# Kernel tuning notes

Hardware: AMD Instinct MI355X
Metric: run time of the kernel (lower is better)

Reference implementation:

```python
import jax, jax.numpy as jnp
import numpy as np

B, T, C = 4, 2048, 2048
H, N = 32, 64          # num_heads, head_size
EPS = 1e-5 * 8.0 ** 2  # GroupNorm eps = 1e-5 * head_size_divisor**2


def setup_inputs() -> dict:
    key = jax.random.key(0)
    ks = jax.random.split(key, 20)
    f = lambda i, shape, s=0.02: jax.random.normal(ks[i], shape, jnp.float32) * s
    return {
        'hidden': jax.random.normal(ks[0], (B, T, C), jnp.float32),
        'time_maa_x': f(1, (C,)), 'time_maa_w': f(2, (C,)), 'time_maa_k': f(3, (C,)),
        'time_maa_v': f(4, (C,)), 'time_maa_r': f(5, (C,)), 'time_maa_g': f(6, (C,)),
        'time_maa_w1': f(7, (C, 160)), 'time_maa_w2': f(8, (5, 32, C)),
        'time_decay': f(9, (C,), 0.5), 'time_decay_w1': f(10, (C, 64)),
        'time_decay_w2': f(11, (64, C)),
        'time_faaaa': f(12, (H, N), 0.5),
        'w_r': f(13, (C, C)), 'w_k': f(14, (C, C)), 'w_v': f(15, (C, C)),
        'w_g': f(16, (C, C)), 'w_o': f(17, (C, C)),
        'ln_w': jnp.ones((C,), jnp.float32), 'ln_b': jnp.zeros((C,), jnp.float32),
    }


def reference(hidden, time_maa_x, time_maa_w, time_maa_k, time_maa_v, time_maa_r,
              time_maa_g, time_maa_w1, time_maa_w2, time_decay, time_decay_w1,
              time_decay_w2, time_faaaa, w_r, w_k, w_v, w_g, w_o, ln_w, ln_b):
    x = hidden
    # time_shift: prepend zero row, drop last (state=None path)
    shifted = jnp.pad(x, ((0, 0), (1, 0), (0, 0)))[:, :-1]
    xx = shifted - x
    # data-dependent low-rank token-shift interpolation (5 lerp channels)
    xm = x + xx * time_maa_x
    t5 = jnp.tanh(jnp.einsum('btc,ce->bte', xm, time_maa_w1)).reshape(B, T, 5, 32)
    m = jnp.einsum('btfe,fec->fbtc', t5, time_maa_w2)  # [5,B,T,C]
    mw, mk, mv, mr, mg = m[0], m[1], m[2], m[3], m[4]
    xd = x + xx * (time_maa_w + mw)
    xk = x + xx * (time_maa_k + mk)
    xv = x + xx * (time_maa_v + mv)
    xr = x + xx * (time_maa_r + mr)
    xg = x + xx * (time_maa_g + mg)
    r = xr @ w_r.T
    k = xk @ w_k.T
    v = xv @ w_v.T
    g = jax.nn.silu(xg @ w_g.T)
    td = time_decay + jnp.tanh(xd @ time_decay_w1) @ time_decay_w2  # [B,T,C]
    w = jnp.exp(-jnp.exp(td))  # per-channel decay in (0,1)
    # [B,T,C] -> [T,B,H,N] for the scan
    to_tbhn = lambda a: a.reshape(B, T, H, N).transpose(1, 0, 2, 3)
    rT, kT, vT, wT = to_tbhn(r), to_tbhn(k), to_tbhn(v), to_tbhn(w)
    u = time_faaaa  # [H,N]
    state0 = jnp.zeros((B, H, N, N), jnp.float32)  # [B,H,key,value]

    def step(state, ins):
        r_t, k_t, v_t, w_t = ins  # each [B,H,N]
        att = k_t[..., :, None] * v_t[..., None, :]        # outer product k v^T
        out_t = jnp.einsum('bhn,bhnm->bhm', r_t,
                           u[None, :, :, None] * att + state)
        new_state = att + w_t[..., None] * state           # decay along key dim
        return new_state, out_t

    _, outs = jax.lax.scan(step, state0, (rT, kT, vT, wT))  # outs [T,B,H,N]
    out = outs.transpose(1, 0, 2, 3)                         # [B,T,H,N]
    # GroupNorm with H groups over C channels, applied per (b,t) sample
    mu = out.mean(-1, keepdims=True)
    var = out.var(-1, keepdims=True)
    out = (out - mu) / jnp.sqrt(var + EPS)
    out = (out * ln_w.reshape(H, N) + ln_b.reshape(H, N)).reshape(B, T, C)
    out = out * g
    return out @ w_o.T
```

## Files before the change

kernel.cpp:

```cpp
#include <hip/hip_runtime.h>
#include <hip/hip_bf16.h>
#include <math.h>

typedef __hip_bfloat16 bf16;
typedef __attribute__((ext_vector_type(8))) short short8;
typedef __attribute__((ext_vector_type(4))) float f32x4;

#define Bb 4
#define Tt 2048
#define Cc 2048
#define Hh 32
#define Nn 64
#define BT (Bb*Tt)
#define Gg 16
#define Ll 128
#define SPLITK 8

__device__ __forceinline__ float b2f(bf16 x) { return __bfloat162float(x); }
__device__ __forceinline__ bf16  f2b(float x) { return __float2bfloat16(x); }

__global__ __launch_bounds__(256) void cvt_kernel(
    const float* __restrict__ in, bf16* __restrict__ out)
{
  int i = blockIdx.x * 256 + threadIdx.x;
  out[i] = f2b(in[i]);
}

__global__ __launch_bounds__(256) void cvt_t2_kernel(
    const float* __restrict__ in, bf16* __restrict__ hi, bf16* __restrict__ lo,
    int N)
{
  int idx = blockIdx.x * 256 + threadIdx.x;
  int n = idx >> 11, k = idx & 2047;
  float v = in[(size_t)k * N + n];
  bf16 h = f2b(v);
  hi[idx] = h;
  lo[idx] = f2b(v - b2f(h));
}

__global__ __launch_bounds__(256) void prep_xm_kernel(
    const float* __restrict__ x, const float* __restrict__ maa_x,
    bf16* __restrict__ xm)
{
  int idx = blockIdx.x * 256 + threadIdx.x;
  int c  = idx & (Cc - 1);
  int bt = idx >> 11;
  int t  = bt & (Tt - 1);
  float xv   = x[idx];
  float prev = (t == 0) ? 0.f : x[idx - Cc];
  xm[idx] = f2b(xv + (prev - xv) * maa_x[c]);
}

#define LDA 40

__global__ __launch_bounds__(256) void mfma_gemm_kernel(
    const bf16* __restrict__ A, const bf16* __restrict__ B,
    bf16* __restrict__ outB, float* __restrict__ outF, int mode)
{
  __shared__ bf16 As[128 * LDA];
  __shared__ bf16 Bs[128 * LDA];
  int tid  = threadIdx.x;
  int lane = tid & 63, wid = tid >> 6;
  int wm = wid & 1, wn = wid >> 1;
  int quad = lane >> 4, l16 = lane & 15;
  size_t rowBase = (size_t)blockIdx.x * 128;
  size_t colBase = (size_t)blockIdx.y * 128;

  f32x4 acc[4][4];
  #pragma unroll
  for (int i = 0; i < 4; ++i)
    #pragma unroll
    for (int j = 0; j < 4; ++j)
      acc[i][j] = (f32x4){0.f, 0.f, 0.f, 0.f};

  for (int k0 = 0; k0 < 2048; k0 += 32) {
    #pragma unroll
    for (int pass = 0; pass < 2; ++pass) {
      int chunk = tid + pass * 256;
      int row = chunk >> 2, kc = (chunk & 3) * 8;
      short8 av = *(const short8*)(A + (rowBase + row) * 2048 + k0 + kc);
      short8 bv = *(const short8*)(B + (colBase + row) * 2048 + k0 + kc);
      *(short8*)(As + row * LDA + kc) = av;
      *(short8*)(Bs + row * LDA + kc) = bv;
    }
    __syncthreads();
    short8 af[4], bf[4];
    #pragma unroll
    for (int i = 0; i < 4; ++i) {
      af[i] = *(const short8*)(As + (wm * 64 + i * 16 + l16) * LDA + quad * 8);
      bf[i] = *(const short8*)(Bs + (wn * 64 + i * 16 + l16) * LDA + quad * 8);
    }
    #pragma unroll
    for (int i = 0; i < 4; ++i)
      #pragma unroll
      for (int j = 0; j < 4; ++j)
        acc[i][j] = __builtin_amdgcn_mfma_f32_16x16x32_bf16(af[i], bf[j], acc[i][j], 0, 0, 0);
    __syncthreads();
  }

  #pragma unroll
  for (int i = 0; i < 4; ++i) {
    #pragma unroll
    for (int j = 0; j < 4; ++j) {
      int gc = colBase + wn * 64 + j * 16 + l16;
      #pragma unroll
      for (int reg = 0; reg < 4; ++reg) {
        int gr = rowBase + wm * 64 + i * 16 + quad * 4 + reg;
        float v = acc[i][j][reg];
        size_t idx = (size_t)gr * 2048 + gc;
        if (mode == 0)      outB[idx] = f2b(v);
        else if (mode == 2) outB[idx] = f2b(v / (1.f + expf(-v)));
        else                outF[idx] = v;
      }
    }
  }
}

template<int NF>
__global__ __launch_bounds__(256) void mfma_skinny_kernel(
    const bf16* __restrict__ A, const bf16* __restrict__ Bt_hi,
    const bf16* __restrict__ Bt_lo,
    float* __restrict__ partial, int kseg_len)
{
  constexpr int N = NF * 16;
  __shared__ bf16 As[64 * LDA];
  __shared__ bf16 Bs[2 * N * LDA];
  int tid = threadIdx.x;
  int lane = tid & 63, w = tid >> 6;
  int quad = lane >> 4, l16 = lane & 15;
  int rowBase = blockIdx.x * 64;
  int kbeg = blockIdx.y * kseg_len;

  f32x4 acc[NF];
  #pragma unroll
  for (int f = 0; f < NF; ++f) acc[f] = (f32x4){0.f, 0.f, 0.f, 0.f};

  for (int k0 = kbeg; k0 < kbeg + kseg_len; k0 += 32) {
    {
      int row = tid >> 2, kc = (tid & 3) * 8;
      *(short8*)(As + row * LDA + kc) =
          *(const short8*)(A + (size_t)(rowBase + row) * 2048 + k0 + kc);
    }
    for (int c = tid; c < N * 8; c += 256) {
      int half = c >= N * 4;
      int cc = c - half * N * 4;
      int row = cc >> 2, kc = (cc & 3) * 8;
      const bf16* src = half ? Bt_lo : Bt_hi;
      *(short8*)(Bs + (half * N + row) * LDA + kc) =
          *(const short8*)(src + (size_t)row * 2048 + k0 + kc);
    }
    __syncthreads();
    short8 af = *(const short8*)(As + (w * 16 + l16) * LDA + quad * 8);
    #pragma unroll
    for (int f = 0; f < NF; ++f) {
      short8 bh = *(const short8*)(Bs + (f * 16 + l16) * LDA + quad * 8);
      short8 bl = *(const short8*)(Bs + ((N + f * 16 + l16)) * LDA + quad * 8);
      acc[f] = __builtin_amdgcn_mfma_f32_16x16x32_bf16(af, bh, acc[f], 0, 0, 0);
      acc[f] = __builtin_amdgcn_mfma_f32_16x16x32_bf16(af, bl, acc[f], 0, 0, 0);
    }
    __syncthreads();
  }

  #pragma unroll
  for (int f = 0; f < NF; ++f) {
    int gc = f * 16 + l16;
    #pragma unroll
    for (int reg = 0; reg < 4; ++reg) {
      int gr = rowBase + w * 16 + quad * 4 + reg;
      partial[((size_t)blockIdx.y * 8192 + gr) * N + gc] = acc[f][reg];
    }
  }
}

__global__ __launch_bounds__(256) void reduce_tanh_kernel(
    const float* __restrict__ partial, bf16* __restrict__ out, int MN)
{
  int idx = blockIdx.x * 256 + threadIdx.x;
  float s = 0.f;
  #pragma unroll
  for (int j = 0; j < SPLITK; ++j) s += partial[(size_t)j * MN + idx];
  out[idx] = f2b(tanhf(s));
}

#define BM 128
#define BN 128
#define BKk 16

__global__ __launch_bounds__(256) void gemm_kernel(
    const bf16* __restrict__ A, const float* __restrict__ Bm,
    bf16* __restrict__ outB,
    const float* __restrict__ bias,
    int M, int N, int K, int transB, int mode)
{
  __shared__ float As[BKk][BM + 1];
  __shared__ float Bs[BKk][BN + 1];
  int tid = threadIdx.x;
  int rowBase = blockIdx.x * BM;
  int colBase = blockIdx.y * BN;
  int tx = tid & 15, ty = tid >> 4;
  float acc[8][8];
  #pragma unroll
  for (int i = 0; i < 8; ++i)
    #pragma unroll
    for (int j = 0; j < 8; ++j) acc[i][j] = 0.f;

  for (int k0 = 0; k0 < K; k0 += BKk) {
    #pragma unroll
    for (int i = 0; i < 8; ++i) {
      int lin = tid + i * 256;
      int r = lin >> 4, kk = lin & 15;
      int gr = rowBase + r, gk = k0 + kk;
      float val = 0.f;
      if (gr < M && gk < K) val = b2f(A[(size_t)gr * K + gk]);
      As[kk][r] = val;
    }
    #pragma unroll
    for (int i = 0; i < 8; ++i) {
      int lin = tid + i * 256;
      float val = 0.f;
      if (transB) {
        int n = lin >> 4, kk = lin & 15;
        int gn = colBase + n, gk = k0 + kk;
        if (gn < N && gk < K) val = Bm[(size_t)gn * K + gk];
        Bs[kk][n] = val;
      } else {
        int kk = lin >> 7, n = lin & 127;
        int gn = colBase + n, gk = k0 + kk;
        if (gn < N && gk < K) val = Bm[(size_t)gk * N + gn];
        Bs[kk][n] = val;
      }
    }
    __syncthreads();
    #pragma unroll
    for (int kk = 0; kk < BKk; ++kk) {
      float a[8], b[8];
      #pragma unroll
      for (int i = 0; i < 8; ++i) a[i] = As[kk][ty * 8 + i];
      #pragma unroll
      for (int j = 0; j < 8; ++j) b[j] = Bs[kk][tx * 8 + j];
      #pragma unroll
      for (int i = 0; i < 8; ++i)
        #pragma unroll
        for (int j = 0; j < 8; ++j)
          acc[i][j] = fmaf(a[i], b[j], acc[i][j]);
    }
    __syncthreads();
  }
  #pragma unroll
  for (int i = 0; i < 8; ++i) {
    int gr = rowBase + ty * 8 + i;
    if (gr >= M) continue;
    #pragma unroll
    for (int j = 0; j < 8; ++j) {
      int gn = colBase + tx * 8 + j;
      if (gn >= N) continue;
      float v = acc[i][j];
      size_t idx = (size_t)gr * N + gn;
      if (mode == 1)      outB[idx] = f2b(tanhf(v));
      else                outB[idx] = f2b(bias[gn] + v);
    }
  }
}

__global__ __launch_bounds__(256) void lerp5_kernel(
    const float* __restrict__ x, const bf16* __restrict__ t5,
    const float* __restrict__ w2,
    const float* __restrict__ maa_w, const float* __restrict__ maa_k,
    const float* __restrict__ maa_v, const float* __restrict__ maa_r,
    const float* __restrict__ maa_g,
    bf16* __restrict__ xd, bf16* __restrict__ xk, bf16* __restrict__ xv_,
    bf16* __restrict__ xr, bf16* __restrict__ xg)
{
  __shared__ float t5s[160];
  int bt   = blockIdx.x >> 3;
  int cblk = blockIdx.x & 7;
  int c = cblk * 256 + threadIdx.x;
  if (threadIdx.x < 160) t5s[threadIdx.x] = b2f(t5[(size_t)bt * 160 + threadIdx.x]);
  __syncthreads();
  int t = bt & (Tt - 1);
  size_t idx = (size_t)bt * Cc + c;
  float xv0  = x[idx];
  float prev = (t == 0) ? 0.f : x[idx - Cc];
  float xx = prev - xv0;
  float m[5];
  #pragma unroll
  for (int f = 0; f < 5; ++f) {
    float s = 0.f;
    #pragma unroll
    for (int e = 0; e < 32; ++e)
      s = fmaf(t5s[f * 32 + e], w2[(size_t)(f * 32 + e) * Cc + c], s);
    m[f] = s;
  }
  xd[idx]  = f2b(xv0 + xx * (maa_w[c] + m[0]));
  xk[idx]  = f2b(xv0 + xx * (maa_k[c] + m[1]));
  xv_[idx] = f2b(xv0 + xx * (maa_v[c] + m[2]));
  xr[idx]  = f2b(xv0 + xx * (maa_r[c] + m[3]));
  xg[idx]  = f2b(xv0 + xx * (maa_g[c] + m[4]));
}

__global__ __launch_bounds__(256) void wkv_local_kernel(
    const bf16* __restrict__ k, const bf16* __restrict__ v,
    const bf16* __restrict__ td,
    float* __restrict__ S_local, float* __restrict__ wp)
{
  int bh = blockIdx.x >> 4;
  int c  = blockIdx.x & 15;
  int b  = bh >> 5, h = bh & 31;
  int tid = threadIdx.x;
  int m = tid & 63, chunk = tid >> 6;
  __shared__ float kw[2][64][2];
  __shared__ float vsb[2][64];
  float s[16], wpr[16];
  #pragma unroll
  for (int i = 0; i < 16; ++i) { s[i] = 0.f; wpr[i] = 1.f; }
  size_t base = (size_t)b * Tt * Cc + (size_t)(c * Ll) * Cc + (size_t)h * 64;
  for (int t = 0; t < Ll; ++t, base += Cc) {
    int p = t & 1;
    int role = tid >> 6, ch = tid & 63;
    if (role == 0)      kw[p][ch][0] = b2f(k[base + ch]);
    else if (role == 1) kw[p][ch][1] = expf(-expf(b2f(td[base + ch])));
    else if (role == 2) vsb[p][ch]   = b2f(v[base + ch]);
    __syncthreads();
    float vm = vsb[p][m];
    #pragma unroll
    for (int i = 0; i < 16; ++i) {
      float kk = kw[p][chunk * 16 + i][0];
      float ww = kw[p][chunk * 16 + i][1];
      s[i] = fmaf(ww, s[i], kk * vm);
      wpr[i] *= ww;
    }
  }
  size_t sb = ((size_t)blockIdx.x * 64 + chunk * 16) * 64 + m;
  #pragma unroll
  for (int i = 0; i < 16; ++i) S_local[sb + (size_t)i * 64] = s[i];
  if (m == 0) {
    int wb = blockIdx.x * 64 + chunk * 16;
    #pragma unroll
    for (int i = 0; i < 16; ++i) wp[wb + i] = wpr[i];
  }
}

__global__ __launch_bounds__(256) void wkv_combine_kernel(
    const float* __restrict__ S_local, const float* __restrict__ wp,
    float* __restrict__ S_start)
{
  int idx = blockIdx.x * 256 + threadIdx.x;
  int m = idx & 63;
  int n = (idx >> 6) & 63;
  int bh = idx >> 12;
  float cur = 0.f;
  #pragma unroll
  for (int c = 0; c < Gg; ++c) {
    size_t sbase = (((size_t)(bh * Gg + c)) * 64 + n) * 64 + m;
    S_start[sbase] = cur;
    cur = fmaf(wp[(bh * Gg + c) * 64 + n], cur, S_local[sbase]);
  }
}

__global__ __launch_bounds__(256) void wkv_out_kernel(
    const bf16* __restrict__ r, const bf16* __restrict__ k,
    const bf16* __restrict__ v, const bf16* __restrict__ td,
    const float* __restrict__ u, const float* __restrict__ S_start,
    bf16* __restrict__ out)
{
  int bh = blockIdx.x >> 4;
  int c  = blockIdx.x & 15;
  int b  = bh >> 5, h = bh & 31;
  int tid = threadIdx.x;
  int m = tid & 63, chunk = tid >> 6;
  __shared__ float4 rkw[64];
  __shared__ float vsb[64];
  __shared__ float red[256];
  float s[16], ureg[16];
  size_t sb = ((size_t)blockIdx.x * 64 + chunk * 16) * 64 + m;
  #pragma unroll
  for (int i = 0; i < 16; ++i) {
    s[i]    = S_start[sb + (size_t)i * 64];
    ureg[i] = u[h * 64 + chunk * 16 + i];
  }
  size_t base = (size_t)b * Tt * Cc + (size_t)(c * Ll) * Cc + (size_t)h * 64;
  for (int t = 0; t < Ll; ++t, base += Cc) {
    int role = tid >> 6, ch = tid & 63;
    if (role == 0)      rkw[ch].x = b2f(r[base + ch]);
    else if (role == 1) rkw[ch].y = b2f(k[base + ch]);
    else if (role == 2) rkw[ch].z = expf(-expf(b2f(td[base + ch])));
    else                vsb[ch]   = b2f(v[base + ch]);
    __syncthreads();
    float vm = vsb[m];
    float acc = 0.f;
    #pragma unroll
    for (int i = 0; i < 16; ++i) {
      float4 q = rkw[chunk * 16 + i];
      float kv = q.y * vm;
      acc = fmaf(q.x, fmaf(ureg[i], kv, s[i]), acc);
      s[i] = fmaf(q.z, s[i], kv);
    }
    red[tid] = acc;
    __syncthreads();
    if (tid < 64)
      out[base + tid] = f2b(red[tid] + red[tid + 64] + red[tid + 128] + red[tid + 192]);
  }
}

__global__ __launch_bounds__(256) void gn_gate_kernel(
    const bf16* __restrict__ wkv, const bf16* __restrict__ g,
    const float* __restrict__ lnw, const float* __restrict__ lnb,
    bf16* __restrict__ out)
{
  int bt = blockIdx.x;
  int wv = threadIdx.x >> 6, lane = threadIdx.x & 63;
  const float EPS = 6.4e-4f;
  for (int h = wv; h < Hh; h += 4) {
    size_t base = (size_t)bt * Cc + h * 64;
    float x = b2f(wkv[base + lane]);
    float s = x, s2 = x * x;
    #pragma unroll
    for (int off = 1; off < 64; off <<= 1) {
      s  += __shfl_xor(s, off);
      s2 += __shfl_xor(s2, off);
    }
    float mean = s * (1.f / 64.f);
    float var  = s2 * (1.f / 64.f) - mean * mean;
    float inv  = rsqrtf(var + EPS);
    float normed = (x - mean) * inv * lnw[h * 64 + lane] + lnb[h * 64 + lane];
    out[base + lane] = f2b(normed * b2f(g[base + lane]));
  }
}

extern "C" void kernel_launch(void* const* d_in, const int* in_sizes, int n_in,
                              void* d_out, int out_size, void* d_ws, size_t ws_size,
                              hipStream_t stream) {
  const float* hidden = (const float*)d_in[0];
  const float* maa_x  = (const float*)d_in[1];
  const float* maa_w  = (const float*)d_in[2];
  const float* maa_k  = (const float*)d_in[3];
  const float* maa_v  = (const float*)d_in[4];
  const float* maa_r  = (const float*)d_in[5];
  const float* maa_g  = (const float*)d_in[6];
  const float* maa_w1 = (const float*)d_in[7];
  const float* maa_w2 = (const float*)d_in[8];
  const float* tdecay = (const float*)d_in[9];
  const float* dw1    = (const float*)d_in[10];
  const float* dw2    = (const float*)d_in[11];
  const float* faaaa  = (const float*)d_in[12];
  const float* w_r    = (const float*)d_in[13];
  const float* w_k    = (const float*)d_in[14];
  const float* w_v    = (const float*)d_in[15];
  const float* w_g    = (const float*)d_in[16];
  const float* w_o    = (const float*)d_in[17];
  const float* lnw    = (const float*)d_in[18];
  const float* lnb    = (const float*)d_in[19];
  float* outF = (float*)d_out;
  bf16* rscratch = (bf16*)d_out;

  char* ws = (char*)d_ws;
  const size_t BUF  = (size_t)BT * Cc * sizeof(bf16);
  const size_t WBUF = (size_t)Cc * Cc * sizeof(bf16);
  const size_t MB = 1024 * 1024;
  bf16* buf0 = (bf16*)(ws + 0 * BUF);
  bf16* buf1 = (bf16*)(ws + 1 * BUF);
  bf16* buf2 = (bf16*)(ws + 2 * BUF);
  bf16* buf3 = (bf16*)(ws + 3 * BUF);
  bf16* buf4 = (bf16*)(ws + 4 * BUF);
  char* small = ws + 5 * BUF;
  bf16* t5buf   = (bf16*)(small + 0);
  bf16* abuf    = (bf16*)(small + 4 * MB);
  bf16* w1t_hi  = (bf16*)(small + 5 * MB);
  bf16* w1t_lo  = (bf16*)(small + 5 * MB + 768 * 1024);
  bf16* dw1t_hi = (bf16*)(small + 6 * MB + 512 * 1024);
  bf16* dw1t_lo = (bf16*)(small + 6 * MB + 768 * 1024);
  char* wbase = small + 8 * MB;
  bf16* wrb = (bf16*)(wbase + 0 * WBUF);
  bf16* wkb = (bf16*)(wbase + 1 * WBUF);
  bf16* wvb = (bf16*)(wbase + 2 * WBUF);
  bf16* wgb = (bf16*)(wbase + 3 * WBUF);
  bf16* wob = (bf16*)(wbase + 4 * WBUF);

  float* slbuf = (float*)((char*)d_out + BUF);
  float* ssbuf = (float*)buf0;
  float* wpbuf = (float*)t5buf;
  float* pbuf  = (float*)d_out;

  dim3 blk(256);
  const int CVT_G = Cc * Cc / 256;

  cvt_kernel<<<dim3(CVT_G), blk, 0, stream>>>(w_r, wrb);
  cvt_kernel<<<dim3(CVT_G), blk, 0, stream>>>(w_k, wkb);
  cvt_kernel<<<dim3(CVT_G), blk, 0, stream>>>(w_v, wvb);
  cvt_kernel<<<dim3(CVT_G), blk, 0, stream>>>(w_g, wgb);
  cvt_kernel<<<dim3(CVT_G), blk, 0, stream>>>(w_o, wob);
  cvt_t2_kernel<<<dim3(160 * Cc / 256), blk, 0, stream>>>(maa_w1, w1t_hi, w1t_lo, 160);
  cvt_t2_kernel<<<dim3(64 * Cc / 256), blk, 0, stream>>>(dw1, dw1t_hi, dw1t_lo, 64);

  prep_xm_kernel<<<dim3(BT * Cc / 256), blk, 0, stream>>>(hidden, maa_x, buf0);

  mfma_skinny_kernel<10><<<dim3(128, SPLITK), blk, 0, stream>>>(
      buf0, w1t_hi, w1t_lo, pbuf, 2048 / SPLITK);
  reduce_tanh_kernel<<<dim3(BT * 160 / 256), blk, 0, stream>>>(pbuf, t5buf,
                                                               BT * 160);

  lerp5_kernel<<<dim3(BT * 8), blk, 0, stream>>>(hidden, t5buf, maa_w2,
      maa_w, maa_k, maa_v, maa_r, maa_g, buf1, buf2, buf3, buf4, buf0);

  mfma_skinny_kernel<4><<<dim3(128, SPLITK), blk, 0, stream>>>(
      buf1, dw1t_hi, dw1t_lo, pbuf, 2048 / SPLITK);
  reduce_tanh_kernel<<<dim3(BT * 64 / 256), blk, 0, stream>>>(pbuf, abuf,
                                                              BT * 64);
  gemm_kernel<<<dim3(64, 16), blk, 0, stream>>>(abuf, dw2, buf1, tdecay,
                                                BT, Cc, 64, 0, 3);

  mfma_gemm_kernel<<<dim3(64, 16), blk, 0, stream>>>(buf4, wrb, rscratch, nullptr, 0);
  mfma_gemm_kernel<<<dim3(64, 16), blk, 0, stream>>>(buf2, wkb, buf4, nullptr, 0);
  mfma_gemm_kernel<<<dim3(64, 16), blk, 0, stream>>>(buf3, wvb, buf2, nullptr, 0);
  mfma_gemm_kernel<<<dim3(64, 16), blk, 0, stream>>>(buf0, wgb, buf3, nullptr, 2);

  wkv_local_kernel<<<dim3(Bb * Hh * Gg), blk, 0, stream>>>(buf4, buf2, buf1,
                                                           slbuf, wpbuf);
  wkv_combine_kernel<<<dim3(Bb * Hh * Nn * Nn / 256), blk, 0, stream>>>(
      slbuf, wpbuf, ssbuf);
  wkv_out_kernel<<<dim3(Bb * Hh * Gg), blk, 0, stream>>>(rscratch, buf4, buf2,
      buf1, faaaa, ssbuf, buf1);

  gn_gate_kernel<<<dim3(BT), blk, 0, stream>>>(buf1, buf3, lnw, lnb, buf4);

  mfma_gemm_kernel<<<dim3(64, 16), blk, 0, stream>>>(buf4, wob, nullptr, outF, 4);
}
```

Before: 1.909 ms.

## Compute lerp5 low-rank projection with MFMA tiles using split-bf16 weights

Replaces the scalar per-thread 160-term dot product in lerp5 with a tiled MFMA kernel. The maa_w2 weights are pre-transposed and split into hi/lo bf16 parts so accuracy stays close to fp32, and the lerp epilogue is fused into the tile output. The aim is to remove the scalar FMA and strided weight-load cost of the old kernel. In exchange it adds a conversion kernel and uses scratch space inside the output buffer. Its epilogue stores are strided per lane, which may be less coalesced than before.

```diff
diff --git a/kernel.cpp b/kernel.cpp
--- a/kernel.cpp
+++ b/kernel.cpp
@@ -33,6 +33,17 @@
   int idx = blockIdx.x * 256 + threadIdx.x;
   int n = idx >> 11, k = idx & 2047;
   float v = in[(size_t)k * N + n];
+  bf16 h = f2b(v);
+  hi[idx] = h;
+  lo[idx] = f2b(v - b2f(h));
+}
+
+__global__ __launch_bounds__(256) void cvt_w2t_kernel(
+    const float* __restrict__ in, bf16* __restrict__ hi, bf16* __restrict__ lo)
+{
+  int idx = blockIdx.x * 256 + threadIdx.x;
+  int c = idx / 160, e = idx - c * 160;
+  float v = in[(size_t)e * Cc + c];
   bf16 h = f2b(v);
   hi[idx] = h;
   lo[idx] = f2b(v - b2f(h));
@@ -262,40 +273,71 @@
   }
 }
 
-__global__ __launch_bounds__(256) void lerp5_kernel(
+__global__ __launch_bounds__(256) void lerp5_mfma_kernel(
     const float* __restrict__ x, const bf16* __restrict__ t5,
-    const float* __restrict__ w2,
+    const bf16* __restrict__ w2t_hi, const bf16* __restrict__ w2t_lo,
     const float* __restrict__ maa_w, const float* __restrict__ maa_k,
     const float* __restrict__ maa_v, const float* __restrict__ maa_r,
     const float* __restrict__ maa_g,
     bf16* __restrict__ xd, bf16* __restrict__ xk, bf16* __restrict__ xv_,
     bf16* __restrict__ xr, bf16* __restrict__ xg)
 {
-  __shared__ float t5s[160];
-  int bt   = blockIdx.x >> 3;
-  int cblk = blockIdx.x & 7;
-  int c = cblk * 256 + threadIdx.x;
-  if (threadIdx.x < 160) t5s[threadIdx.x] = b2f(t5[(size_t)bt * 160 + threadIdx.x]);
-  __syncthreads();
-  int t = bt & (Tt - 1);
-  size_t idx = (size_t)bt * Cc + c;
-  float xv0  = x[idx];
-  float prev = (t == 0) ? 0.f : x[idx - Cc];
-  float xx = prev - xv0;
-  float m[5];
+  int tid  = threadIdx.x;
+  int lane = tid & 63, wid = tid >> 6;
+  int wm = wid & 1, wn = wid >> 1;
+  int quad = lane >> 4, l16 = lane & 15;
+  int rowBase = blockIdx.x * 128;
+  int colBase = blockIdx.y * 128;
+
+  const float* maas[5] = {maa_w, maa_k, maa_v, maa_r, maa_g};
+  bf16* outs[5] = {xd, xk, xv_, xr, xg};
+
   #pragma unroll
   for (int f = 0; f < 5; ++f) {
-    float s = 0.f;
-    #pragma unroll
-    for (int e = 0; e < 32; ++e)
-      s = fmaf(t5s[f * 32 + e], w2[(size_t)(f * 32 + e) * Cc + c], s);
-    m[f] = s;
-  }
-  xd[idx]  = f2b(xv0 + xx * (maa_w[c] + m[0]));
-  xk[idx]  = f2b(xv0 + xx * (maa_k[c] + m[1]));
-  xv_[idx] = f2b(xv0 + xx * (maa_v[c] + m[2]));
-  xr[idx]  = f2b(xv0 + xx * (maa_r[c] + m[3]));
-  xg[idx]  = f2b(xv0 + xx * (maa_g[c] + m[4]));
+    short8 af[4];
+    #pragma unroll
+    for (int i = 0; i < 4; ++i)
+      af[i] = *(const short8*)(t5 +
+          (size_t)(rowBase + wm * 64 + i * 16 + l16) * 160 + f * 32 + quad * 8);
+
+    f32x4 acc[4][4];
+    #pragma unroll
+    for (int i = 0; i < 4; ++i)
+      #pragma unroll
+      for (int j = 0; j < 4; ++j)
+        acc[i][j] = (f32x4){0.f, 0.f, 0.f, 0.f};
+
+    #pragma unroll
+    for (int j = 0; j < 4; ++j) {
+      size_t boff = (size_t)(colBase + wn * 64 + j * 16 + l16) * 160 + f * 32 + quad * 8;
+      short8 bh = *(const short8*)(w2t_hi + boff);
+      short8 bl = *(const short8*)(w2t_lo + boff);
+      #pragma unroll
+      for (int i = 0; i < 4; ++i) {
+        acc[i][j] = __builtin_amdgcn_mfma_f32_16x16x32_bf16(af[i], bh, acc[i][j], 0, 0, 0);
+        acc[i][j] = __builtin_amdgcn_mfma_f32_16x16x32_bf16(af[i], bl, acc[i][j], 0, 0, 0);
+      }
+    }
+
+    const float* maa = maas[f];
+    bf16* outp = outs[f];
+    #pragma unroll
+    for (int j = 0; j < 4; ++j) {
+      int gc = colBase + wn * 64 + j * 16 + l16;
+      float mv = maa[gc];
+      #pragma unroll
+      for (int i = 0; i < 4; ++i) {
+        #pragma unroll
+        for (int reg = 0; reg < 4; ++reg) {
+          int gr = rowBase + wm * 64 + i * 16 + quad * 4 + reg;
+          size_t idx = (size_t)gr * Cc + gc;
+          float xv0  = x[idx];
+          float prev = ((gr & (Tt - 1)) == 0) ? 0.f : x[idx - Cc];
+          outp[idx] = f2b(xv0 + (prev - xv0) * (mv + acc[i][j][reg]));
+        }
+      }
+    }
+  }
 }
 
 __global__ __launch_bounds__(256) void wkv_local_kernel(
@@ -476,6 +518,9 @@
   bf16* wgb = (bf16*)(wbase + 3 * WBUF);
   bf16* wob = (bf16*)(wbase + 4 * WBUF);
 
+  bf16* w2t_hi = (bf16*)((char*)d_out + 48 * MB);
+  bf16* w2t_lo = (bf16*)((char*)d_out + 49 * MB);
+
   float* slbuf = (float*)((char*)d_out + BUF);
   float* ssbuf = (float*)buf0;
   float* wpbuf = (float*)t5buf;
@@ -491,6 +536,7 @@
   cvt_kernel<<<dim3(CVT_G), blk, 0, stream>>>(w_o, wob);
   cvt_t2_kernel<<<dim3(160 * Cc / 256), blk, 0, stream>>>(maa_w1, w1t_hi, w1t_lo, 160);
   cvt_t2_kernel<<<dim3(64 * Cc / 256), blk, 0, stream>>>(dw1, dw1t_hi, dw1t_lo, 64);
+  cvt_w2t_kernel<<<dim3(160 * Cc / 256), blk, 0, stream>>>(maa_w2, w2t_hi, w2t_lo);
 
   prep_xm_kernel<<<dim3(BT * Cc / 256), blk, 0, stream>>>(hidden, maa_x, buf0);
 
@@ -499,8 +545,9 @@
   reduce_tanh_kernel<<<dim3(BT * 160 / 256), blk, 0, stream>>>(pbuf, t5buf,
                                                                BT * 160);
 
-  lerp5_kernel<<<dim3(BT * 8), blk, 0, stream>>>(hidden, t5buf, maa_w2,
-      maa_w, maa_k, maa_v, maa_r, maa_g, buf1, buf2, buf3, buf4, buf0);
+  lerp5_mfma_kernel<<<dim3(64, 16), blk, 0, stream>>>(hidden, t5buf,
+      w2t_hi, w2t_lo, maa_w, maa_k, maa_v, maa_r, maa_g,
+      buf1, buf2, buf3, buf4, buf0);
 
   mfma_skinny_kernel<4><<<dim3(128, SPLITK), blk, 0, stream>>>(
       buf1, dw1t_hi, dw1t_lo, pbuf, 2048 / SPLITK);
```

Measured after the change: 1.830 ms. 1.04x faster.
